# Optimization experiments

Hardware: AMD Instinct MI355X
Metric: run time of the kernel (lower is better)

## Reference

```python
import jax, jax.numpy as jnp
import numpy as np

EMBED = 768
HEADS = 12
FACTOR = 2
LN_EPS = 1e-5


def layer_norm(x, gamma, beta):
    mu = jnp.mean(x, axis=-1, keepdims=True)
    var = jnp.mean(jnp.square(x - mu), axis=-1, keepdims=True)
    return (x - mu) * jax.lax.rsqrt(var + LN_EPS) * gamma + beta


def setup_inputs() -> dict:
    key = jax.random.key(0)
    ks = jax.random.split(key, 8)
    B, S, E = 8, 1024, EMBED
    H = FACTOR * E
    s_e = 1.0 / np.sqrt(E)
    s_h = 1.0 / np.sqrt(H)
    return {
        "x": jax.random.normal(ks[0], (B, S, E), jnp.float32),
        "Wq": jax.random.normal(ks[1], (E, E), jnp.float32) * s_e,
        "Wk": jax.random.normal(ks[2], (E, E), jnp.float32) * s_e,
        "Wv": jax.random.normal(ks[3], (E, E), jnp.float32) * s_e,
        "W1": jax.random.normal(ks[4], (E, H), jnp.float32) * s_e,
        "b1": jnp.zeros((H,), jnp.float32),
        "W2": jax.random.normal(ks[5], (H, E), jnp.float32) * s_h,
        "b2": jnp.zeros((E,), jnp.float32),
        "g1": jnp.ones((E,), jnp.float32),
        "beta1": jnp.zeros((E,), jnp.float32),
        "g2": jnp.ones((E,), jnp.float32),
        "beta2": jnp.zeros((E,), jnp.float32),
    }


def reference(x, Wq, Wk, Wv, W1, b1, W2, b2, g1, beta1, g2, beta2):
    B, S, E = x.shape
    hd = E // HEADS
    # NOTE: original reshapes (B,S,E)->(B,H,S,hd) WITHOUT transposing heads
    # (non-standard: mixes sequence blocks across heads) - replicated faithfully.
    q = (x @ Wq).reshape(B, HEADS, S, hd)
    k = (x @ Wk).reshape(B, HEADS, S, hd)
    v = (x @ Wv).reshape(B, HEADS, S, hd)
    # no 1/sqrt(d) scaling in the original
    attn = jax.nn.softmax(jnp.einsum('bnqd,bnkd->bnqk', q, k), axis=-1)
    # NOTE: original einsum 'bnqk,bnvd->bnqd' sums over BOTH k and v
    # (value is sum-pooled over its sequence axis) - replicated faithfully.
    out = jnp.einsum('bnqk,bnvd->bnqd', attn, v)
    out = out.transpose(0, 2, 1, 3).reshape(B, S, E)
    a = x + layer_norm(out, g1, beta1)
    # GELU after BOTH linears (exact GELU, torch default)
    h = jax.nn.gelu(a @ W1 + b1, approximate=False)
    m = jax.nn.gelu(h @ W2 + b2, approximate=False)
    return x + layer_norm(m, g2, beta2)
```

## Files before the change

### kernel.cpp

```cpp
#include <hip/hip_runtime.h>
#include <hip/hip_bf16.h>
#include <math.h>

#define E_ 768
#define HID_ 1536
#define SQ_ 1024

typedef unsigned short u16;
using bf16x8 = __attribute__((ext_vector_type(8))) __bf16;
using f32x4  = __attribute__((ext_vector_type(4))) float;

__device__ __forceinline__ u16 f2bf(float f) {
  union { float f; unsigned u; } v; v.f = f;
  unsigned r = v.u + 0x7FFFu + ((v.u >> 16) & 1u);
  return (u16)(r >> 16);
}
__device__ __forceinline__ float bf2f(u16 h) {
  union { unsigned u; float f; } v; v.u = ((unsigned)h) << 16; return v.f;
}
__device__ __forceinline__ float gelu_f(float x) {
  return 0.5f * x * (1.0f + erff(x * 0.70710678118654752f));
}

#define GLDS16(gp, sp) __builtin_amdgcn_global_load_lds( \
    (__attribute__((address_space(1))) const void*)(const void*)(gp), \
    (__attribute__((address_space(3))) void*)(void*)(sp), 16, 0, 0)

__global__ void prep_kernel(const float* __restrict__ x, const float* __restrict__ W1,
                            const float* __restrict__ W2, u16* __restrict__ xb,
                            u16* __restrict__ W1T, u16* __restrict__ W2T) {
  __shared__ float T[64 * 65];
  int bid = blockIdx.x, t = threadIdx.x;
  if (bid < 6144) {
    int base = bid * 1024 + t * 4;
    const float4 v = *reinterpret_cast<const float4*>(x + base);
    ushort4 o; o.x = f2bf(v.x); o.y = f2bf(v.y); o.z = f2bf(v.z); o.w = f2bf(v.w);
    *reinterpret_cast<ushort4*>(xb + base) = o;
    return;
  }
  const float* in; u16* out; int R_in, C_in, rt, ct;
  if (bid < 6432) {
    int b2 = bid - 6144; in = W1; out = W1T; R_in = 768; C_in = 1536;
    rt = b2 / 24; ct = b2 % 24;
  } else {
    int b3 = bid - 6432; in = W2; out = W2T; R_in = 1536; C_in = 768;
    rt = b3 / 12; ct = b3 % 12;
  }
  int r0 = rt << 6, c0 = ct << 6;
  int tr = t >> 4, tc4 = (t & 15) << 2;
#pragma unroll
  for (int i = 0; i < 4; ++i) {
    int row = tr + (i << 4);
    const float4 v = *reinterpret_cast<const float4*>(in + (size_t)(r0 + row) * C_in + c0 + tc4);
    T[row * 65 + tc4 + 0] = v.x;
    T[row * 65 + tc4 + 1] = v.y;
    T[row * 65 + tc4 + 2] = v.z;
    T[row * 65 + tc4 + 3] = v.w;
  }
  __syncthreads();
#pragma unroll
  for (int i = 0; i < 4; ++i) {
    int orow = tr + (i << 4);
    ushort4 o;
    o.x = f2bf(T[(tc4 + 0) * 65 + orow]);
    o.y = f2bf(T[(tc4 + 1) * 65 + orow]);
    o.z = f2bf(T[(tc4 + 2) * 65 + orow]);
    o.w = f2bf(T[(tc4 + 3) * 65 + orow]);
    *reinterpret_cast<ushort4*>(out + (size_t)(c0 + orow) * R_in + r0 + tc4) = o;
  }
}

__global__ void rowsum_kernel(const u16* __restrict__ xb, float* __restrict__ Rp) {
  int bid = blockIdx.x;
  int r = bid >> 2, c = bid & 3;
  int b = r / 12, n = r % 12;
  int t = threadIdx.x;
  int u0 = n << 10;
  int s_lo = u0 / 12;
  int s_hi = (u0 + 1023) / 12;
  int cnt = s_hi - s_lo + 1;
  int cs = s_lo + (cnt * c) / 4;
  int ce = s_lo + (cnt * (c + 1)) / 4;
  float acc[12][3];
#pragma unroll
  for (int g = 0; g < 12; ++g)
    for (int q = 0; q < 3; ++q) acc[g][q] = 0.f;
  const u16* xp = xb + (size_t)b * SQ_ * E_;
  for (int s = cs; s < ce; ++s) {
    float v0 = bf2f(xp[(size_t)s * E_ + t]);
    float v1 = bf2f(xp[(size_t)s * E_ + t + 256]);
    float v2 = bf2f(xp[(size_t)s * E_ + t + 512]);
    int du = 12 * s - u0;
#pragma unroll
    for (int g = 0; g < 12; ++g) {
      int u = du + g;
      if (u >= 0 && u < 1024) { acc[g][0] += v0; acc[g][1] += v1; acc[g][2] += v2; }
    }
  }
  float* Rr = Rp + (size_t)bid * 9216;
#pragma unroll
  for (int g = 0; g < 12; ++g) {
    Rr[g * 768 + t]       = acc[g][0];
    Rr[g * 768 + t + 256] = acc[g][1];
    Rr[g * 768 + t + 512] = acc[g][2];
  }
}

__global__ void ygemm_kernel(const float* __restrict__ Rp, const float* __restrict__ Wv,
                             float* __restrict__ P3) {
  int g = blockIdx.x, r = blockIdx.y, jc = blockIdx.z;
  int t = threadIdx.x;
  int d = t & 63, sub = t >> 6;
  const float* R0 = Rp + (size_t)r * 4 * 9216 + g * 768;
  const float* wp = Wv + g * 64 + d;
  int j0 = jc * 96 + sub * 24;
  float a0 = 0.f, a1 = 0.f, a2 = 0.f, a3 = 0.f;
#pragma unroll
  for (int jj = 0; jj < 24; jj += 4) {
    int j = j0 + jj;
    float r0v = R0[j + 0] + R0[9216 + j + 0] + R0[18432 + j + 0] + R0[27648 + j + 0];
    float r1v = R0[j + 1] + R0[9216 + j + 1] + R0[18432 + j + 1] + R0[27648 + j + 1];
    float r2v = R0[j + 2] + R0[9216 + j + 2] + R0[18432 + j + 2] + R0[27648 + j + 2];
    float r3v = R0[j + 3] + R0[9216 + j + 3] + R0[18432 + j + 3] + R0[27648 + j + 3];
    a0 += r0v * wp[(size_t)(j + 0) * 768];
    a1 += r1v * wp[(size_t)(j + 1) * 768];
    a2 += r2v * wp[(size_t)(j + 2) * 768];
    a3 += r3v * wp[(size_t)(j + 3) * 768];
  }
  __shared__ float red[256];
  red[t] = (a0 + a1) + (a2 + a3);
  __syncthreads();
  if (sub == 0)
    P3[(((size_t)r * 12 + g) * 8 + jc) * 64 + d] = red[d] + red[64 + d] + red[128 + d] + red[192 + d];
}

__global__ void ysum_kernel(const float* __restrict__ P3, float* __restrict__ Y) {
  int bn = blockIdx.x;
  int t = threadIdx.x;
  int d = t & 63, sub = t >> 6;
  const float* Pp = P3 + (size_t)bn * 6144 + d;
  int g0 = sub * 24;
  float s = 0.f;
#pragma unroll 8
  for (int gj = 0; gj < 24; ++gj) s += Pp[(g0 + gj) << 6];
  __shared__ float red[256];
  red[t] = s;
  __syncthreads();
  if (sub == 0)
    Y[bn * 64 + d] = red[d] + red[64 + d] + red[128 + d] + red[192 + d];
}

__global__ void ln1_kernel(const float* __restrict__ Y, const float* __restrict__ g1,
                           const float* __restrict__ be1, float* __restrict__ L1) {
  int b = blockIdx.x, t = threadIdx.x;
  float y0 = Y[b * 768 + t];
  float y1 = Y[b * 768 + t + 256];
  float y2 = Y[b * 768 + t + 512];
  float s = y0 + y1 + y2;
  float sq = y0 * y0 + y1 * y1 + y2 * y2;
  __shared__ float red[8];
#pragma unroll
  for (int o = 32; o > 0; o >>= 1) { s += __shfl_down(s, o, 64); sq += __shfl_down(sq, o, 64); }
  if ((t & 63) == 0) { red[(t >> 6) * 2] = s; red[(t >> 6) * 2 + 1] = sq; }
  __syncthreads();
  s  = red[0] + red[2] + red[4] + red[6];
  sq = red[1] + red[3] + red[5] + red[7];
  float mu = s * (1.f / 768.f);
  float var = sq * (1.f / 768.f) - mu * mu;
  float rs = rsqrtf(var + 1e-5f);
  L1[b * 768 + t]       = (y0 - mu) * rs * g1[t]       + be1[t];
  L1[b * 768 + t + 256] = (y1 - mu) * rs * g1[t + 256] + be1[t + 256];
  L1[b * 768 + t + 512] = (y2 - mu) * rs * g1[t + 512] + be1[t + 512];
}

__global__ void c1_kernel(const float* __restrict__ L1, const float* __restrict__ W1,
                          const float* __restrict__ b1, float* __restrict__ C1) {
  int bid = blockIdx.x;
  int b = bid / 48, c = bid % 48;
  int t = threadIdx.x;
  __shared__ float Ls[768];
  __shared__ float red[8][32];
  for (int q = t; q < 768; q += 256) Ls[q] = L1[b * 768 + q];
  __syncthreads();
  int tc = t & 31, ts = t >> 5;
  int n = c * 32 + tc;
  float acc = 0.f;
  int j0 = ts * 96;
#pragma unroll 4
  for (int j = j0; j < j0 + 96; ++j) acc += Ls[j] * W1[(size_t)j * HID_ + n];
  red[ts][tc] = acc;
  __syncthreads();
  if (ts == 0) {
    float s = b1[n];
#pragma unroll
    for (int k = 0; k < 8; ++k) s += red[k][tc];
    C1[b * HID_ + n] = s;
  }
}

template <int MODE>
__global__ __launch_bounds__(256, 3) void gemm_bt_kernel(
    const u16* __restrict__ A, const u16* __restrict__ BT,
    const float* __restrict__ bias, void* __restrict__ out0, void* __restrict__ out1,
    int N, int lda, int ldb) {
  __shared__ __align__(16) u16 As[128 * 64];
  __shared__ __align__(16) u16 Bs[128 * 64];
  int bid = blockIdx.x;
  int xcd = bid & 7, idx = bid >> 3;
  int mloc, n_, k_off, kk = 0;
  if (MODE == 0) { mloc = idx / 12; n_ = idx % 12; k_off = 0; }
  else           { kk = idx / 48; int rem = idx % 48; mloc = rem / 6; n_ = rem % 6; k_off = kk * 768; }
  int bm = (xcd * 8 + mloc) << 7, bn = n_ << 7;

  int t = threadIdx.x;
  int lane = t & 63, w = t >> 6;
  int wm = (w >> 1) << 6, wn = (w & 1) << 6;
  int quad = lane >> 4, l16 = lane & 15;
  f32x4 acc[4][4] = {};

  for (int k0 = 0; k0 < 768; k0 += 64) {
    __syncthreads();
#pragma unroll
    for (int i = 0; i < 4; ++i) {
      int ci = t + (i << 8);
      int r = ci >> 3, csw = ci & 7;
      int kc = csw ^ (r & 7);
      const u16* ga = A + (size_t)(bm + r) * lda + k_off + k0 + (kc << 3);
      GLDS16(ga, As + ci * 8);
      const u16* gb = BT + (size_t)(bn + r) * ldb + k_off + k0 + (kc << 3);
      GLDS16(gb, Bs + ci * 8);
    }
    __builtin_amdgcn_s_waitcnt(0);
    __syncthreads();
#pragma unroll
    for (int ks = 0; ks < 2; ++ks) {
      bf16x8 af[4], bf[4];
      int kc = (ks << 2) + quad;
#pragma unroll
      for (int mt = 0; mt < 4; ++mt) {
        int row = wm + (mt << 4) + l16;
        af[mt] = *reinterpret_cast<const bf16x8*>(As + row * 64 + ((kc ^ (row & 7)) << 3));
      }
#pragma unroll
      for (int nt = 0; nt < 4; ++nt) {
        int row = wn + (nt << 4) + l16;
        bf[nt] = *reinterpret_cast<const bf16x8*>(Bs + row * 64 + ((kc ^ (row & 7)) << 3));
      }
#pragma unroll
      for (int mt = 0; mt < 4; ++mt)
#pragma unroll
        for (int nt = 0; nt < 4; ++nt)
          acc[mt][nt] = __builtin_amdgcn_mfma_f32_16x16x32_bf16(af[mt], bf[nt], acc[mt][nt], 0, 0, 0);
    }
  }

#pragma unroll
  for (int mt = 0; mt < 4; ++mt) {
    int row0 = bm + wm + (mt << 4) + (quad << 2);
#pragma unroll
    for (int nt = 0; nt < 4; ++nt) {
      int col = bn + wn + (nt << 4) + l16;
      float bv = (MODE == 0) ? bias[(bm >> 10) * N + col] : 0.f;
#pragma unroll
      for (int rr = 0; rr < 4; ++rr) {
        float v = acc[mt][nt][rr] + bv;
        size_t idxo = (size_t)(row0 + rr) * N + col;
        if (MODE == 0)       ((u16*)out0)[idxo] = f2bf(gelu_f(v));
        else if (kk == 0)    ((u16*)out0)[idxo] = f2bf(v);
        else                 ((u16*)out1)[idxo] = f2bf(v);
      }
    }
  }
}

__global__ void ln2_kernel(const u16* __restrict__ p0, const u16* __restrict__ p1,
                           const float* __restrict__ x, const float* __restrict__ b2,
                           const float* __restrict__ g2, const float* __restrict__ be2,
                           float* __restrict__ out) {
  int row = blockIdx.x, t = threadIdx.x;
  int e = t << 2;
  ushort4 pa = *reinterpret_cast<const ushort4*>(p0 + (size_t)row * 768 + e);
  ushort4 pb = *reinterpret_cast<const ushort4*>(p1 + (size_t)row * 768 + e);
  float4 bb = *reinterpret_cast<const float4*>(b2 + e);
  float v0 = gelu_f(bf2f(pa.x) + bf2f(pb.x) + bb.x);
  float v1 = gelu_f(bf2f(pa.y) + bf2f(pb.y) + bb.y);
  float v2 = gelu_f(bf2f(pa.z) + bf2f(pb.z) + bb.z);
  float v3 = gelu_f(bf2f(pa.w) + bf2f(pb.w) + bb.w);
  float s = (v0 + v1) + (v2 + v3);
  float sq = (v0 * v0 + v1 * v1) + (v2 * v2 + v3 * v3);
  __shared__ float red[6];
#pragma unroll
  for (int o = 32; o > 0; o >>= 1) { s += __shfl_down(s, o, 64); sq += __shfl_down(sq, o, 64); }
  if ((t & 63) == 0) { red[(t >> 6) * 2] = s; red[(t >> 6) * 2 + 1] = sq; }
  __syncthreads();
  s  = red[0] + red[2] + red[4];
  sq = red[1] + red[3] + red[5];
  float mu = s * (1.f / 768.f);
  float var = sq * (1.f / 768.f) - mu * mu;
  float rs = rsqrtf(var + 1e-5f);
  float4 gg = *reinterpret_cast<const float4*>(g2 + e);
  float4 be = *reinterpret_cast<const float4*>(be2 + e);
  float4 xx = *reinterpret_cast<const float4*>(x + (size_t)row * 768 + e);
  float4 o;
  o.x = xx.x + (v0 - mu) * rs * gg.x + be.x;
  o.y = xx.y + (v1 - mu) * rs * gg.y + be.y;
  o.z = xx.z + (v2 - mu) * rs * gg.z + be.z;
  o.w = xx.w + (v3 - mu) * rs * gg.w + be.w;
  *reinterpret_cast<float4*>(out + (size_t)row * 768 + e) = o;
}

extern "C" void kernel_launch(void* const* d_in, const int* in_sizes, int n_in,
                              void* d_out, int out_size, void* d_ws, size_t ws_size,
                              hipStream_t stream) {
  const float* x   = (const float*)d_in[0];
  const float* Wv  = (const float*)d_in[3];
  const float* W1  = (const float*)d_in[4];
  const float* b1  = (const float*)d_in[5];
  const float* W2  = (const float*)d_in[6];
  const float* b2  = (const float*)d_in[7];
  const float* g1  = (const float*)d_in[8];
  const float* be1 = (const float*)d_in[9];
  const float* g2  = (const float*)d_in[10];
  const float* be2 = (const float*)d_in[11];
  float* out = (float*)d_out;

  char* ws = (char*)d_ws;
  u16*   xb  = (u16*)(ws);
  u16*   W1T = (u16*)(ws + 12582912);
  u16*   W2T = (u16*)(ws + 14942208);
  u16*   h   = (u16*)(ws + 17301504);
  float* Rp  = (float*)(ws + 17301504);
  float* P3  = (float*)(ws + 42467328);
  float* Y   = (float*)(ws + 44826624);
  float* L1  = (float*)(ws + 44851200);
  float* C1  = (float*)(ws + 44875776);
  u16*   m0  = (u16*)(ws + 44924928);
  u16*   p1  = xb;

  prep_kernel<<<6720, 256, 0, stream>>>(x, W1, W2, xb, W1T, W2T);
  rowsum_kernel<<<384, 256, 0, stream>>>(xb, Rp);
  ygemm_kernel<<<dim3(12, 96, 8), 256, 0, stream>>>(Rp, Wv, P3);
  ysum_kernel<<<96, 256, 0, stream>>>(P3, Y);
  ln1_kernel<<<8, 256, 0, stream>>>(Y, g1, be1, L1);
  c1_kernel<<<384, 256, 0, stream>>>(L1, W1, b1, C1);
  gemm_bt_kernel<0><<<768, 256, 0, stream>>>(xb, W1T, C1, (void*)h, nullptr, 1536, 768, 768);
  gemm_bt_kernel<1><<<768, 256, 0, stream>>>(h, W2T, nullptr, (void*)m0, (void*)p1, 768, 1536, 1536);
  ln2_kernel<<<8192, 192, 0, stream>>>(m0, p1, x, b2, g2, be2, out);
}
```

Baseline: 237.4 us.

## Switch GEMMs to 32x32x16 MFMA, vectorize rowsum, fuse LN1 into c1

The bf16 GEMM kernel now uses 32x32x16 MFMA tiles (2x2 per wave) in place of 16x16x32 tiles (4x4 per wave). This halves the LDS fragment loads per k-step and changes the epilogue store pattern. The rowsum kernel reads ushort4 and writes float4 using 192 threads, and the LayerNorm-1 kernel is folded into c1_kernel, which removes a launch and the L1 round-trip. Each c1 block now recomputes the LayerNorm statistics redundantly, and the epilogue stores are strided differently.

```diff
diff --git a/kernel.cpp b/kernel.cpp
--- a/kernel.cpp
+++ b/kernel.cpp
@@ -8,7 +8,7 @@
 
 typedef unsigned short u16;
 using bf16x8 = __attribute__((ext_vector_type(8))) __bf16;
-using f32x4  = __attribute__((ext_vector_type(4))) float;
+using f32x16 = __attribute__((ext_vector_type(16))) float;
 
 __device__ __forceinline__ u16 f2bf(float f) {
   union { float f; unsigned u; } v; v.f = f;
@@ -81,28 +81,28 @@
   int cnt = s_hi - s_lo + 1;
   int cs = s_lo + (cnt * c) / 4;
   int ce = s_lo + (cnt * (c + 1)) / 4;
-  float acc[12][3];
+  float acc[12][4];
 #pragma unroll
   for (int g = 0; g < 12; ++g)
-    for (int q = 0; q < 3; ++q) acc[g][q] = 0.f;
-  const u16* xp = xb + (size_t)b * SQ_ * E_;
+    for (int q = 0; q < 4; ++q) acc[g][q] = 0.f;
+  const u16* xp = xb + (size_t)b * SQ_ * E_ + (t << 2);
   for (int s = cs; s < ce; ++s) {
-    float v0 = bf2f(xp[(size_t)s * E_ + t]);
-    float v1 = bf2f(xp[(size_t)s * E_ + t + 256]);
-    float v2 = bf2f(xp[(size_t)s * E_ + t + 512]);
+    ushort4 vv = *reinterpret_cast<const ushort4*>(xp + (size_t)s * E_);
+    float v0 = bf2f(vv.x), v1 = bf2f(vv.y), v2 = bf2f(vv.z), v3 = bf2f(vv.w);
     int du = 12 * s - u0;
 #pragma unroll
     for (int g = 0; g < 12; ++g) {
       int u = du + g;
-      if (u >= 0 && u < 1024) { acc[g][0] += v0; acc[g][1] += v1; acc[g][2] += v2; }
+      if (u >= 0 && u < 1024) {
+        acc[g][0] += v0; acc[g][1] += v1; acc[g][2] += v2; acc[g][3] += v3;
+      }
     }
   }
-  float* Rr = Rp + (size_t)bid * 9216;
+  float* Rr = Rp + (size_t)bid * 9216 + (t << 2);
 #pragma unroll
   for (int g = 0; g < 12; ++g) {
-    Rr[g * 768 + t]       = acc[g][0];
-    Rr[g * 768 + t + 256] = acc[g][1];
-    Rr[g * 768 + t + 512] = acc[g][2];
+    float4 o; o.x = acc[g][0]; o.y = acc[g][1]; o.z = acc[g][2]; o.w = acc[g][3];
+    *reinterpret_cast<float4*>(Rr + g * 768) = o;
   }
 }
 
@@ -150,37 +150,32 @@
     Y[bn * 64 + d] = red[d] + red[64 + d] + red[128 + d] + red[192 + d];
 }
 
-__global__ void ln1_kernel(const float* __restrict__ Y, const float* __restrict__ g1,
-                           const float* __restrict__ be1, float* __restrict__ L1) {
-  int b = blockIdx.x, t = threadIdx.x;
+__global__ void c1_kernel(const float* __restrict__ Y, const float* __restrict__ W1,
+                          const float* __restrict__ b1, const float* __restrict__ g1,
+                          const float* __restrict__ be1, float* __restrict__ C1) {
+  int bid = blockIdx.x;
+  int b = bid / 48, c = bid % 48;
+  int t = threadIdx.x;
+  __shared__ float Ls[768];
+  __shared__ float red2[8];
+  __shared__ float red[8][32];
   float y0 = Y[b * 768 + t];
   float y1 = Y[b * 768 + t + 256];
   float y2 = Y[b * 768 + t + 512];
   float s = y0 + y1 + y2;
   float sq = y0 * y0 + y1 * y1 + y2 * y2;
-  __shared__ float red[8];
 #pragma unroll
   for (int o = 32; o > 0; o >>= 1) { s += __shfl_down(s, o, 64); sq += __shfl_down(sq, o, 64); }
-  if ((t & 63) == 0) { red[(t >> 6) * 2] = s; red[(t >> 6) * 2 + 1] = sq; }
-  __syncthreads();
-  s  = red[0] + red[2] + red[4] + red[6];
-  sq = red[1] + red[3] + red[5] + red[7];
+  if ((t & 63) == 0) { red2[(t >> 6) * 2] = s; red2[(t >> 6) * 2 + 1] = sq; }
+  __syncthreads();
+  s  = red2[0] + red2[2] + red2[4] + red2[6];
+  sq = red2[1] + red2[3] + red2[5] + red2[7];
   float mu = s * (1.f / 768.f);
   float var = sq * (1.f / 768.f) - mu * mu;
   float rs = rsqrtf(var + 1e-5f);
-  L1[b * 768 + t]       = (y0 - mu) * rs * g1[t]       + be1[t];
-  L1[b * 768 + t + 256] = (y1 - mu) * rs * g1[t + 256] + be1[t + 256];
-  L1[b * 768 + t + 512] = (y2 - mu) * rs * g1[t + 512] + be1[t + 512];
-}
-
-__global__ void c1_kernel(const float* __restrict__ L1, const float* __restrict__ W1,
-                          const float* __restrict__ b1, float* __restrict__ C1) {
-  int bid = blockIdx.x;
-  int b = bid / 48, c = bid % 48;
-  int t = threadIdx.x;
-  __shared__ float Ls[768];
-  __shared__ float red[8][32];
-  for (int q = t; q < 768; q += 256) Ls[q] = L1[b * 768 + q];
+  Ls[t]       = (y0 - mu) * rs * g1[t]       + be1[t];
+  Ls[t + 256] = (y1 - mu) * rs * g1[t + 256] + be1[t + 256];
+  Ls[t + 512] = (y2 - mu) * rs * g1[t + 512] + be1[t + 512];
   __syncthreads();
   int tc = t & 31, ts = t >> 5;
   int n = c * 32 + tc;
@@ -191,10 +186,10 @@
   red[ts][tc] = acc;
   __syncthreads();
   if (ts == 0) {
-    float s = b1[n];
-#pragma unroll
-    for (int k = 0; k < 8; ++k) s += red[k][tc];
-    C1[b * HID_ + n] = s;
+    float sum = b1[n];
+#pragma unroll
+    for (int k = 0; k < 8; ++k) sum += red[k][tc];
+    C1[b * HID_ + n] = sum;
   }
 }
 
@@ -215,8 +210,8 @@
   int t = threadIdx.x;
   int lane = t & 63, w = t >> 6;
   int wm = (w >> 1) << 6, wn = (w & 1) << 6;
-  int quad = lane >> 4, l16 = lane & 15;
-  f32x4 acc[4][4] = {};
+  int l32 = lane & 31, half = lane >> 5;
+  f32x16 acc[2][2] = {};
 
   for (int k0 = 0; k0 < 768; k0 += 64) {
     __syncthreads();
@@ -233,38 +228,39 @@
     __builtin_amdgcn_s_waitcnt(0);
     __syncthreads();
 #pragma unroll
-    for (int ks = 0; ks < 2; ++ks) {
-      bf16x8 af[4], bf[4];
-      int kc = (ks << 2) + quad;
-#pragma unroll
-      for (int mt = 0; mt < 4; ++mt) {
-        int row = wm + (mt << 4) + l16;
-        af[mt] = *reinterpret_cast<const bf16x8*>(As + row * 64 + ((kc ^ (row & 7)) << 3));
+    for (int kc = 0; kc < 4; ++kc) {
+      int kc2 = (kc << 1) | half;
+      bf16x8 af[2], bf[2];
+#pragma unroll
+      for (int mt = 0; mt < 2; ++mt) {
+        int row = wm + (mt << 5) + l32;
+        af[mt] = *reinterpret_cast<const bf16x8*>(As + row * 64 + ((kc2 ^ (row & 7)) << 3));
       }
 #pragma unroll
-      for (int nt = 0; nt < 4; ++nt) {
-        int row = wn + (nt << 4) + l16;
-        bf[nt] = *reinterpret_cast<const bf16x8*>(Bs + row * 64 + ((kc ^ (row & 7)) << 3));
+      for (int nt = 0; nt < 2; ++nt) {
+        int row = wn + (nt << 5) + l32;
+        bf[nt] = *reinterpret_cast<const bf16x8*>(Bs + row * 64 + ((kc2 ^ (row & 7)) << 3));
       }
 #pragma unroll
-      for (int mt = 0; mt < 4; ++mt)
-#pragma unroll
-        for (int nt = 0; nt < 4; ++nt)
-          acc[mt][nt] = __builtin_amdgcn_mfma_f32_16x16x32_bf16(af[mt], bf[nt], acc[mt][nt], 0, 0, 0);
+      for (int mt = 0; mt < 2; ++mt)
+#pragma unroll
+        for (int nt = 0; nt < 2; ++nt)
+          acc[mt][nt] = __builtin_amdgcn_mfma_f32_32x32x16_bf16(af[mt], bf[nt], acc[mt][nt], 0, 0, 0);
     }
   }
 
 #pragma unroll
-  for (int mt = 0; mt < 4; ++mt) {
-    int row0 = bm + wm + (mt << 4) + (quad << 2);
-#pragma unroll
-    for (int nt = 0; nt < 4; ++nt) {
-      int col = bn + wn + (nt << 4) + l16;
+  for (int mt = 0; mt < 2; ++mt) {
+    int rbase = bm + wm + (mt << 5) + (half << 2);
+#pragma unroll
+    for (int nt = 0; nt < 2; ++nt) {
+      int col = bn + wn + (nt << 5) + l32;
       float bv = (MODE == 0) ? bias[(bm >> 10) * N + col] : 0.f;
 #pragma unroll
-      for (int rr = 0; rr < 4; ++rr) {
-        float v = acc[mt][nt][rr] + bv;
-        size_t idxo = (size_t)(row0 + rr) * N + col;
+      for (int reg = 0; reg < 16; ++reg) {
+        int row = rbase + (reg & 3) + ((reg >> 2) << 3);
+        float v = acc[mt][nt][reg] + bv;
+        size_t idxo = (size_t)row * N + col;
         if (MODE == 0)       ((u16*)out0)[idxo] = f2bf(gelu_f(v));
         else if (kk == 0)    ((u16*)out0)[idxo] = f2bf(v);
         else                 ((u16*)out1)[idxo] = f2bf(v);
@@ -332,17 +328,15 @@
   float* Rp  = (float*)(ws + 17301504);
   float* P3  = (float*)(ws + 42467328);
   float* Y   = (float*)(ws + 44826624);
-  float* L1  = (float*)(ws + 44851200);
   float* C1  = (float*)(ws + 44875776);
   u16*   m0  = (u16*)(ws + 44924928);
   u16*   p1  = xb;
 
   prep_kernel<<<6720, 256, 0, stream>>>(x, W1, W2, xb, W1T, W2T);
-  rowsum_kernel<<<384, 256, 0, stream>>>(xb, Rp);
+  rowsum_kernel<<<384, 192, 0, stream>>>(xb, Rp);
   ygemm_kernel<<<dim3(12, 96, 8), 256, 0, stream>>>(Rp, Wv, P3);
   ysum_kernel<<<96, 256, 0, stream>>>(P3, Y);
-  ln1_kernel<<<8, 256, 0, stream>>>(Y, g1, be1, L1);
-  c1_kernel<<<384, 256, 0, stream>>>(L1, W1, b1, C1);
+  c1_kernel<<<384, 256, 0, stream>>>(Y, W1, b1, g1, be1, C1);
   gemm_bt_kernel<0><<<768, 256, 0, stream>>>(xb, W1T, C1, (void*)h, nullptr, 1536, 768, 768);
   gemm_bt_kernel<1><<<768, 256, 0, stream>>>(h, W2T, nullptr, (void*)m0, (void*)p1, 768, 1536, 1536);
   ln2_kernel<<<8192, 192, 0, stream>>>(m0, p1, x, b2, g2, be2, out);
```

After: 243.8 us. 1.03x slower.
